# Kernel tuning notes

Measured on AMD Instinct MI355X. Metric: run time of the kernel, lower is better.

## Reference

```python
import jax, jax.numpy as jnp
import numpy as np


def setup_inputs() -> dict:
    key = jax.random.key(0)
    ks = jax.random.split(key, 8)
    Bsz, Dm, L, N = 2, 2048, 1024, 16
    u = jax.random.normal(ks[0], (Bsz, Dm, L), jnp.float32)
    delta = jax.random.normal(ks[1], (Bsz, Dm, L), jnp.float32) * 0.5
    # A is negative in Mamba (stable decay); keep values O(1) negative
    A = -jnp.exp(jax.random.normal(ks[2], (Dm, N), jnp.float32) * 0.5)
    B = jax.random.normal(ks[3], (Bsz, N, L), jnp.float32)
    C = jax.random.normal(ks[4], (Bsz, N, L), jnp.float32)
    D = jax.random.normal(ks[5], (Dm,), jnp.float32)
    z = jax.random.normal(ks[6], (Bsz, Dm, L), jnp.float32)
    delta_bias = jax.random.normal(ks[7], (Dm,), jnp.float32) * 0.1
    return {"u": u, "delta": delta, "A": A, "B": B, "C": C,
            "D": D, "z": z, "delta_bias": delta_bias, "delta_softplus": 1}


def reference(u, delta, A, B, C, D, z, delta_bias, delta_softplus):
    # u, delta, z: (Bsz, Dm, L); A: (Dm, N); B, C: (Bsz, N, L)
    dt = delta + delta_bias[None, :, None]
    if delta_softplus:
        dt = jax.nn.softplus(dt)

    # move scan (length) axis to the front
    dt_l = jnp.moveaxis(dt, -1, 0)   # (L, Bsz, Dm)
    u_l = jnp.moveaxis(u, -1, 0)     # (L, Bsz, Dm)
    B_l = jnp.moveaxis(B, -1, 0)     # (L, Bsz, N)
    C_l = jnp.moveaxis(C, -1, 0)     # (L, Bsz, N)

    def step(x, inp):
        dti, ui, Bi, Ci = inp
        dA = jnp.exp(dti[..., None] * A)                  # (Bsz, Dm, N)
        dBu = (dti * ui)[..., None] * Bi[:, None, :]      # (Bsz, Dm, N)
        x = dA * x + dBu
        y = jnp.einsum('bdn,bn->bd', x, Ci)               # (Bsz, Dm)
        return x, y

    x0 = jnp.zeros((u.shape[0], u.shape[1], A.shape[1]), dtype=u.dtype)
    _, ys = jax.lax.scan(step, x0, (dt_l, u_l, B_l, C_l))  # ys: (L, Bsz, Dm)
    y = jnp.moveaxis(ys, 0, -1)                            # (Bsz, Dm, L)
    y = y + u * D[None, :, None]
    y = y * (z * jax.nn.sigmoid(z))  # silu gate
    return y
```

## Files before the change

### kernel.cpp

```cpp
#include <hip/hip_runtime.h>
#include <math.h>

constexpr int Bsz = 2, Dm = 2048, L = 1024, N = 16;
constexpr int CL = 16;
constexpr int WPR = 2;
constexpr int RPB = 4;
constexpr int TPB = RPB * WPR * 64;
constexpr int TI = 2;
constexpr int NT = CL / TI;
constexpr int ISTR2 = 65;
constexpr int LROW2 = CL * ISTR2;
constexpr int TS2 = 8 * 65;
constexpr float LOG2E = 1.4426950408889634f;
constexpr float RLOG2E = 0.6931471805599453f;

#define EXP2(x) __builtin_amdgcn_exp2f(x)

__global__ __launch_bounds__(256) void transform_bc_kernel(
    const float* __restrict__ B_g, const float* __restrict__ C_g,
    float4* __restrict__ Bs, float4* __restrict__ Cs)
{
    const int o = threadIdx.x + 256 * blockIdx.x;
    const int b = blockIdx.y;
    const float* __restrict__ src = blockIdx.z ? C_g : B_g;
    float4* __restrict__ dst = blockIdx.z ? Cs : Bs;
    const int cg = o & 63, k = (o >> 6) & 3, i = o >> 8;
    const int l = cg * CL + i;
    float4 v;
    v.x = src[(size_t)(b * N + 4 * k + 0) * L + l];
    v.y = src[(size_t)(b * N + 4 * k + 1) * L + l];
    v.z = src[(size_t)(b * N + 4 * k + 2) * L + l];
    v.w = src[(size_t)(b * N + 4 * k + 3) * L + l];
    dst[(size_t)b * 4096 + o] = v;
}

template<bool XF>
__global__ __launch_bounds__(TPB) void mamba_scan18_kernel(
    const float* __restrict__ u_g, const float* __restrict__ delta_g,
    const float* __restrict__ A_g,
    const float* __restrict__ B_g, const float* __restrict__ C_g,
    const float4* __restrict__ Bs, const float4* __restrict__ Cs,
    const float* __restrict__ D_g, const float* __restrict__ z_g,
    const float* __restrict__ bias_g, const int* __restrict__ sp_g,
    float* __restrict__ y_g)
{
    __shared__ float2 du_s[RPB * LROW2];
    __shared__ float2 tb2[2][TI * TS2];
    __shared__ float xw_s[RPB][16];

    const int tid = threadIdx.x;
    const int wid = tid >> 6;
    const int lane = tid & 63;
    const int W = wid & 1;
    const int r = wid >> 1;
    const int h = lane >> 5;
    const int c = lane & 31;
    const int cg = W * 32 + c;
    const int row = blockIdx.x * RPB + r;
    const int b = row >> 11;
    const int d = row & (Dm - 1);
    const size_t Bb = (size_t)b * 4096;
    const int lb = r * LROW2;
    const int t128 = tid & 127;
    const int stg0 = (wid >> 2) * TS2 + (2 * (wid & 3)) * 65 + lane;
    const int stg1 = stg0 + 65;
    const int trb = (4 * h) * 65 + cg;

    float4 sB, sC;
    if (XF) sB = Bs[Bb + tid];

#pragma unroll
    for (int p = 0; p < 2; ++p) {
        const int l0 = 4 * t128 + 512 * p;
        const size_t gb = (size_t)row * L + l0;
        const float4 d4 = *reinterpret_cast<const float4*>(&delta_g[gb]);
        const float4 u4 = *reinterpret_cast<const float4*>(&u_g[gb]);
        const float bias = bias_g[d];
        const int sp = sp_g[0];
#pragma unroll
        for (int k = 0; k < 4; ++k) {
            const int li = l0 + k;
            const float t = (&d4.x)[k] + bias;
            const float e = EXP2(-fabsf(t) * LOG2E);
            const float p_ = sp ? (fmaxf(t, 0.f) +
                                   __builtin_amdgcn_logf(1.f + e) * RLOG2E)
                                : t;
            const int a = (li & (CL - 1)) * ISTR2 + (li >> 4);
            du_s[lb + a] = make_float2(p_, (&u4.x)[k]);
        }
    }
    float A2[8];
#pragma unroll
    for (int g = 0; g < 2; ++g) {
        const float4 a4 = *reinterpret_cast<const float4*>(&A_g[d * N + h * 8 + g * 4]);
        A2[g * 4 + 0] = a4.x * LOG2E; A2[g * 4 + 1] = a4.y * LOG2E;
        A2[g * 4 + 2] = a4.z * LOG2E; A2[g * 4 + 3] = a4.w * LOG2E;
    }
    if (XF) {
        tb2[0][stg0] = make_float2(sB.x, sB.y);
        tb2[0][stg1] = make_float2(sB.z, sB.w);
    }
    __syncthreads();

    float x[8], y[8];
#pragma unroll
    for (int n = 0; n < 8; ++n) { x[n] = 0.f; y[n] = 0.f; }
    float ssum = 0.f;

    if (XF) {
#pragma unroll
        for (int t = 0; t < NT; ++t) {
            if (t + 1 < NT) sB = Bs[Bb + (t + 1) * 512 + tid];
#pragma unroll
            for (int il = 0; il < TI; ++il) {
                const int i = t * TI + il;
                const float2 du = du_s[lb + i * ISTR2 + cg];
                const float dtp = du.x;
                const float dtu = du.x * du.y;
                ssum += dtp;
                const int rb = il * TS2 + trb;
                const float2 q0 = tb2[t & 1][rb];
                const float2 q1 = tb2[t & 1][rb + 65];
                const float2 q2 = tb2[t & 1][rb + 130];
                const float2 q3 = tb2[t & 1][rb + 195];
                const float bv[8] = {q0.x, q0.y, q1.x, q1.y,
                                     q2.x, q2.y, q3.x, q3.y};
#pragma unroll
                for (int n = 0; n < 8; ++n) {
                    const float a = EXP2(dtp * A2[n]);
                    x[n] = fmaf(a, x[n], dtu * bv[n]);
                }
            }
            if (t + 1 < NT) {
                tb2[(t + 1) & 1][stg0] = make_float2(sB.x, sB.y);
                tb2[(t + 1) & 1][stg1] = make_float2(sB.z, sB.w);
            }
            __syncthreads();
        }
    } else {
#pragma unroll
        for (int i = 0; i < CL; ++i) {
            const float2 du = du_s[lb + i * ISTR2 + cg];
            const float dtp = du.x;
            const float dtu = du.x * du.y;
            ssum += dtp;
            const int l = cg * CL + i;
            const int k0 = 2 * h;
            float4 B0, B1;
#pragma unroll
            for (int q = 0; q < 4; ++q) {
                (&B0.x)[q] = B_g[(size_t)(b * N + 4 * k0 + q) * L + l];
                (&B1.x)[q] = B_g[(size_t)(b * N + 4 * k0 + 4 + q) * L + l];
            }
            const float bv[8] = {B0.x, B0.y, B0.z, B0.w, B1.x, B1.y, B1.z, B1.w};
#pragma unroll
            for (int n = 0; n < 8; ++n) {
                const float a = EXP2(dtp * A2[n]);
                x[n] = fmaf(a, x[n], dtu * bv[n]);
            }
        }
    }

    if (XF) { sB = Bs[Bb + tid]; sC = Cs[Bb + tid]; }

    float P[8];
#pragma unroll
    for (int n = 0; n < 8; ++n) P[n] = EXP2(A2[n] * ssum);
#pragma unroll
    for (int s = 1; s < 32; s <<= 1) {
        const bool ok = (c >= s);
#pragma unroll
        for (int n = 0; n < 8; ++n) {
            const float xp = __shfl_up(x[n], s, 32);
            const float Pp = __shfl_up(P[n], s, 32);
            if (ok) {
                x[n] = fmaf(P[n], xp, x[n]);
                P[n] = P[n] * Pp;
            }
        }
    }

    if (W == 0 && c == 31) {
#pragma unroll
        for (int n = 0; n < 8; ++n) xw_s[r][h * 8 + n] = x[n];
    }
    if (XF) {
        tb2[0][stg0] = make_float2(sB.x, sB.y);
        tb2[0][stg1] = make_float2(sB.z, sB.w);
        tb2[1][stg0] = make_float2(sC.x, sC.y);
        tb2[1][stg1] = make_float2(sC.z, sC.w);
    }
    __syncthreads();

    float xt[8];
#pragma unroll
    for (int n = 0; n < 8; ++n) xt[n] = xw_s[r][h * 8 + n];
#pragma unroll
    for (int n = 0; n < 8; ++n) {
        const float xi = __shfl_up(x[n], 1, 32);
        const float Pi = __shfl_up(P[n], 1, 32);
        const float xe = (c == 0) ? 0.f : xi;
        const float Pe = (c == 0) ? 1.f : Pi;
        x[n] = W ? fmaf(Pe, xt[n], xe) : xe;
    }

    const float Dd = D_g[d];
    if (XF) {
#pragma unroll
        for (int t = 0; t < NT; ++t) {
            if (t + 1 < NT) {
                sB = Bs[Bb + (t + 1) * 512 + tid];
                sC = Cs[Bb + (t + 1) * 512 + tid];
            }
#pragma unroll
            for (int il = 0; il < TI; ++il) {
                const int i = t * TI + il;
                const float2 du = du_s[lb + i * ISTR2 + cg];
                const float dtp = du.x;
                const float uu = du.y;
                const float dtu = dtp * uu;
                const int rb = il * TS2 + trb;
                const float2 b0 = tb2[0][rb];
                const float2 b1 = tb2[0][rb + 65];
                const float2 b2 = tb2[0][rb + 130];
                const float2 b3 = tb2[0][rb + 195];
                const float2 c0 = tb2[1][rb];
                const float2 c1 = tb2[1][rb + 65];
                const float2 c2 = tb2[1][rb + 130];
                const float2 c3 = tb2[1][rb + 195];
                const float bv[8] = {b0.x, b0.y, b1.x, b1.y,
                                     b2.x, b2.y, b3.x, b3.y};
                const float cv[8] = {c0.x, c0.y, c1.x, c1.y,
                                     c2.x, c2.y, c3.x, c3.y};
                float acc = 0.f;
#pragma unroll
                for (int n = 0; n < 8; ++n) {
                    const float a = EXP2(dtp * A2[n]);
                    x[n] = fmaf(a, x[n], dtu * bv[n]);
                    acc = fmaf(x[n], cv[n], acc);
                }
                acc += __shfl_xor(acc, 32, 64);
                const float yv = fmaf(uu, Dd, acc);
                y[i & 7] = ((i >> 3) == h) ? yv : y[i & 7];
            }
            __syncthreads();
            if (t + 1 < NT) {
                tb2[0][stg0] = make_float2(sB.x, sB.y);
                tb2[0][stg1] = make_float2(sB.z, sB.w);
                tb2[1][stg0] = make_float2(sC.x, sC.y);
                tb2[1][stg1] = make_float2(sC.z, sC.w);
                __syncthreads();
            }
        }
    } else {
#pragma unroll
        for (int i = 0; i < CL; ++i) {
            const float2 du = du_s[lb + i * ISTR2 + cg];
            const float dtp = du.x;
            const float uu = du.y;
            const float dtu = dtp * uu;
            const int l = cg * CL + i;
            const int k0 = 2 * h;
            float4 B0, B1, C0, C1;
#pragma unroll
            for (int q = 0; q < 4; ++q) {
                (&B0.x)[q] = B_g[(size_t)(b * N + 4 * k0 + q) * L + l];
                (&B1.x)[q] = B_g[(size_t)(b * N + 4 * k0 + 4 + q) * L + l];
                (&C0.x)[q] = C_g[(size_t)(b * N + 4 * k0 + q) * L + l];
                (&C1.x)[q] = C_g[(size_t)(b * N + 4 * k0 + 4 + q) * L + l];
            }
            const float bv[8] = {B0.x, B0.y, B0.z, B0.w, B1.x, B1.y, B1.z, B1.w};
            const float cv[8] = {C0.x, C0.y, C0.z, C0.w, C1.x, C1.y, C1.z, C1.w};
            float acc = 0.f;
#pragma unroll
            for (int n = 0; n < 8; ++n) {
                const float a = EXP2(dtp * A2[n]);
                x[n] = fmaf(a, x[n], dtu * bv[n]);
                acc = fmaf(x[n], cv[n], acc);
            }
            acc += __shfl_xor(acc, 32, 64);
            const float yv = fmaf(uu, Dd, acc);
            y[i & 7] = ((i >> 3) == h) ? yv : y[i & 7];
        }
    }

    {
        const size_t gz = (size_t)row * L + cg * CL + h * 8;
        const float4 z0 = *reinterpret_cast<const float4*>(&z_g[gz]);
        const float4 z1 = *reinterpret_cast<const float4*>(&z_g[gz + 4]);
        float out[8];
#pragma unroll
        for (int j = 0; j < 8; ++j) {
            const float zv = (j < 4) ? (&z0.x)[j] : (&z1.x)[j - 4];
            const float e = EXP2(-zv * LOG2E);
            const float sig = __builtin_amdgcn_rcpf(1.f + e);
            out[j] = y[j] * (zv * sig);
        }
        *reinterpret_cast<float4*>(&y_g[gz]) =
            make_float4(out[0], out[1], out[2], out[3]);
        *reinterpret_cast<float4*>(&y_g[gz + 4]) =
            make_float4(out[4], out[5], out[6], out[7]);
    }
}

extern "C" void kernel_launch(void* const* d_in, const int* in_sizes, int n_in,
                              void* d_out, int out_size, void* d_ws, size_t ws_size,
                              hipStream_t stream) {
    const float* u     = (const float*)d_in[0];
    const float* delta = (const float*)d_in[1];
    const float* A     = (const float*)d_in[2];
    const float* B     = (const float*)d_in[3];
    const float* C     = (const float*)d_in[4];
    const float* D     = (const float*)d_in[5];
    const float* z     = (const float*)d_in[6];
    const float* bias  = (const float*)d_in[7];
    const int*   sp    = (const int*)d_in[8];
    float* y = (float*)d_out;

    const size_t bc_bytes = (size_t)Bsz * 4096 * sizeof(float4);
    const bool xf = ws_size >= 2 * bc_bytes;
    float4* Bs = (float4*)d_ws;
    float4* Cs = (float4*)((char*)d_ws + bc_bytes);

    if (xf) {
        transform_bc_kernel<<<dim3(16, Bsz, 2), 256, 0, stream>>>(B, C, Bs, Cs);
        mamba_scan18_kernel<true><<<dim3((Bsz * Dm) / RPB), TPB, 0, stream>>>(
            u, delta, A, B, C, Bs, Cs, D, z, bias, sp, y);
    } else {
        mamba_scan18_kernel<false><<<dim3((Bsz * Dm) / RPB), TPB, 0, stream>>>(
            u, delta, A, B, C, Bs, Cs, D, z, bias, sp, y);
    }
}
```

Measured before the change: 49.58 us.

## Deepen B/C prefetch pipeline and replace syncthreads with lightweight LDS barrier

Restructures the staging of the transformed B/C tiles so global loads are issued two steps ahead in registers and written into a double-buffered LDS tile, with one barrier per step instead of two. The second pass now stages B and C per timestep using half the threads each, rather than all threads loading both. A custom barrier that waits only on LDS counters (not global loads) replaces __syncthreads, so outstanding prefetches are not forced to complete at each barrier. The trade-off is more barriers in the output pass (one per timestep instead of per two) and more live registers for the prefetch buffers.

Measured after the change: 49.37 us. About the same (-0.4%).

```diff
diff --git a/kernel.cpp b/kernel.cpp
--- a/kernel.cpp
+++ b/kernel.cpp
@@ -6,8 +6,7 @@
 constexpr int WPR = 2;
 constexpr int RPB = 4;
 constexpr int TPB = RPB * WPR * 64;
-constexpr int TI = 2;
-constexpr int NT = CL / TI;
+constexpr int NT = 8;
 constexpr int ISTR2 = 65;
 constexpr int LROW2 = CL * ISTR2;
 constexpr int TS2 = 8 * 65;
@@ -15,6 +14,12 @@
 constexpr float RLOG2E = 0.6931471805599453f;
 
 #define EXP2(x) __builtin_amdgcn_exp2f(x)
+
+__device__ __forceinline__ void wg_barrier() {
+    asm volatile("s_waitcnt lgkmcnt(0)" ::: "memory");
+    __builtin_amdgcn_s_barrier();
+    asm volatile("" ::: "memory");
+}
 
 __global__ __launch_bounds__(256) void transform_bc_kernel(
     const float* __restrict__ B_g, const float* __restrict__ C_g,
@@ -35,7 +40,7 @@
 }
 
 template<bool XF>
-__global__ __launch_bounds__(TPB) void mamba_scan18_kernel(
+__global__ __launch_bounds__(TPB) void mamba_scan19_kernel(
     const float* __restrict__ u_g, const float* __restrict__ delta_g,
     const float* __restrict__ A_g,
     const float* __restrict__ B_g, const float* __restrict__ C_g,
@@ -45,7 +50,7 @@
     float* __restrict__ y_g)
 {
     __shared__ float2 du_s[RPB * LROW2];
-    __shared__ float2 tb2[2][TI * TS2];
+    __shared__ float2 tb2[2][2 * TS2];
     __shared__ float xw_s[RPB][16];
 
     const int tid = threadIdx.x;
@@ -64,29 +69,36 @@
     const int t128 = tid & 127;
     const int stg0 = (wid >> 2) * TS2 + (2 * (wid & 3)) * 65 + lane;
     const int stg1 = stg0 + 65;
+    const int bc = tid >> 8;
+    const int t256 = tid & 255;
+    const int pstg0 = bc * TS2 + (2 * ((t256 >> 6) & 3)) * 65 + (t256 & 63);
+    const int pstg1 = pstg0 + 65;
+    const float4* __restrict__ psrc = (bc ? Cs : Bs) + Bb;
     const int trb = (4 * h) * 65 + cg;
 
-    float4 sB, sC;
-    if (XF) sB = Bs[Bb + tid];
-
-#pragma unroll
-    for (int p = 0; p < 2; ++p) {
-        const int l0 = 4 * t128 + 512 * p;
-        const size_t gb = (size_t)row * L + l0;
-        const float4 d4 = *reinterpret_cast<const float4*>(&delta_g[gb]);
-        const float4 u4 = *reinterpret_cast<const float4*>(&u_g[gb]);
+    float4 s0, s1;
+    if (XF) s0 = Bs[Bb + tid];
+
+    {
         const float bias = bias_g[d];
         const int sp = sp_g[0];
 #pragma unroll
-        for (int k = 0; k < 4; ++k) {
-            const int li = l0 + k;
-            const float t = (&d4.x)[k] + bias;
-            const float e = EXP2(-fabsf(t) * LOG2E);
-            const float p_ = sp ? (fmaxf(t, 0.f) +
-                                   __builtin_amdgcn_logf(1.f + e) * RLOG2E)
-                                : t;
-            const int a = (li & (CL - 1)) * ISTR2 + (li >> 4);
-            du_s[lb + a] = make_float2(p_, (&u4.x)[k]);
+        for (int p = 0; p < 2; ++p) {
+            const int l0 = 4 * t128 + 512 * p;
+            const size_t gb = (size_t)row * L + l0;
+            const float4 d4 = *reinterpret_cast<const float4*>(&delta_g[gb]);
+            const float4 u4 = *reinterpret_cast<const float4*>(&u_g[gb]);
+#pragma unroll
+            for (int k = 0; k < 4; ++k) {
+                const int li = l0 + k;
+                const float t = (&d4.x)[k] + bias;
+                const float e = EXP2(-fabsf(t) * LOG2E);
+                const float p_ = sp ? (fmaxf(t, 0.f) +
+                                       __builtin_amdgcn_logf(1.f + e) * RLOG2E)
+                                    : t;
+                const int a = (li & (CL - 1)) * ISTR2 + (li >> 4);
+                du_s[lb + a] = make_float2(p_, (&u4.x)[k]);
+            }
         }
     }
     float A2[8];
@@ -97,10 +109,12 @@
         A2[g * 4 + 2] = a4.z * LOG2E; A2[g * 4 + 3] = a4.w * LOG2E;
     }
     if (XF) {
-        tb2[0][stg0] = make_float2(sB.x, sB.y);
-        tb2[0][stg1] = make_float2(sB.z, sB.w);
-    }
-    __syncthreads();
+        tb2[0][stg0] = make_float2(s0.x, s0.y);
+        tb2[0][stg1] = make_float2(s0.z, s0.w);
+        s0 = Bs[Bb + 512 + tid];
+        s1 = Bs[Bb + 1024 + tid];
+    }
+    wg_barrier();
 
     float x[8], y[8];
 #pragma unroll
@@ -110,10 +124,9 @@
     if (XF) {
 #pragma unroll
         for (int t = 0; t < NT; ++t) {
-            if (t + 1 < NT) sB = Bs[Bb + (t + 1) * 512 + tid];
-#pragma unroll
-            for (int il = 0; il < TI; ++il) {
-                const int i = t * TI + il;
+#pragma unroll
+            for (int il = 0; il < 2; ++il) {
+                const int i = 2 * t + il;
                 const float2 du = du_s[lb + i * ISTR2 + cg];
                 const float dtp = du.x;
                 const float dtu = du.x * du.y;
@@ -132,10 +145,15 @@
                 }
             }
             if (t + 1 < NT) {
-                tb2[(t + 1) & 1][stg0] = make_float2(sB.x, sB.y);
-                tb2[(t + 1) & 1][stg1] = make_float2(sB.z, sB.w);
-            }
-            __syncthreads();
+                const float4 sv = (t & 1) ? s1 : s0;
+                tb2[(t + 1) & 1][stg0] = make_float2(sv.x, sv.y);
+                tb2[(t + 1) & 1][stg1] = make_float2(sv.z, sv.w);
+            }
+            if (t + 3 < NT) {
+                if (t & 1) s1 = Bs[Bb + (t + 3) * 512 + tid];
+                else       s0 = Bs[Bb + (t + 3) * 512 + tid];
+            }
+            if (t + 1 < NT) wg_barrier();
         }
     } else {
 #pragma unroll
@@ -161,7 +179,8 @@
         }
     }
 
-    if (XF) { sB = Bs[Bb + tid]; sC = Cs[Bb + tid]; }
+    float4 p0, p1;
+    if (XF) p0 = psrc[t256];
 
     float P[8];
 #pragma unroll
@@ -185,12 +204,12 @@
         for (int n = 0; n < 8; ++n) xw_s[r][h * 8 + n] = x[n];
     }
     if (XF) {
-        tb2[0][stg0] = make_float2(sB.x, sB.y);
-        tb2[0][stg1] = make_float2(sB.z, sB.w);
-        tb2[1][stg0] = make_float2(sC.x, sC.y);
-        tb2[1][stg1] = make_float2(sC.z, sC.w);
-    }
-    __syncthreads();
+        tb2[0][pstg0] = make_float2(p0.x, p0.y);
+        tb2[0][pstg1] = make_float2(p0.z, p0.w);
+        p0 = psrc[1 * 256 + t256];
+        p1 = psrc[2 * 256 + t256];
+    }
+    wg_barrier();
 
     float xt[8];
 #pragma unroll
@@ -207,50 +226,41 @@
     const float Dd = D_g[d];
     if (XF) {
 #pragma unroll
-        for (int t = 0; t < NT; ++t) {
-            if (t + 1 < NT) {
-                sB = Bs[Bb + (t + 1) * 512 + tid];
-                sC = Cs[Bb + (t + 1) * 512 + tid];
-            }
-#pragma unroll
-            for (int il = 0; il < TI; ++il) {
-                const int i = t * TI + il;
-                const float2 du = du_s[lb + i * ISTR2 + cg];
-                const float dtp = du.x;
-                const float uu = du.y;
-                const float dtu = dtp * uu;
-                const int rb = il * TS2 + trb;
-                const float2 b0 = tb2[0][rb];
-                const float2 b1 = tb2[0][rb + 65];
-                const float2 b2 = tb2[0][rb + 130];
-                const float2 b3 = tb2[0][rb + 195];
-                const float2 c0 = tb2[1][rb];
-                const float2 c1 = tb2[1][rb + 65];
-                const float2 c2 = tb2[1][rb + 130];
-                const float2 c3 = tb2[1][rb + 195];
-                const float bv[8] = {b0.x, b0.y, b1.x, b1.y,
-                                     b2.x, b2.y, b3.x, b3.y};
-                const float cv[8] = {c0.x, c0.y, c1.x, c1.y,
-                                     c2.x, c2.y, c3.x, c3.y};
-                float acc = 0.f;
-#pragma unroll
-                for (int n = 0; n < 8; ++n) {
-                    const float a = EXP2(dtp * A2[n]);
-                    x[n] = fmaf(a, x[n], dtu * bv[n]);
-                    acc = fmaf(x[n], cv[n], acc);
-                }
-                acc += __shfl_xor(acc, 32, 64);
-                const float yv = fmaf(uu, Dd, acc);
-                y[i & 7] = ((i >> 3) == h) ? yv : y[i & 7];
-            }
-            __syncthreads();
-            if (t + 1 < NT) {
-                tb2[0][stg0] = make_float2(sB.x, sB.y);
-                tb2[0][stg1] = make_float2(sB.z, sB.w);
-                tb2[1][stg0] = make_float2(sC.x, sC.y);
-                tb2[1][stg1] = make_float2(sC.z, sC.w);
-                __syncthreads();
-            }
+        for (int i = 0; i < CL; ++i) {
+            const float2 du = du_s[lb + i * ISTR2 + cg];
+            const float dtp = du.x;
+            const float uu = du.y;
+            const float dtu = dtp * uu;
+            const float2 b0 = tb2[i & 1][trb];
+            const float2 b1 = tb2[i & 1][trb + 65];
+            const float2 b2 = tb2[i & 1][trb + 130];
+            const float2 b3 = tb2[i & 1][trb + 195];
+            const float2 c0 = tb2[i & 1][TS2 + trb];
+            const float2 c1 = tb2[i & 1][TS2 + trb + 65];
+            const float2 c2 = tb2[i & 1][TS2 + trb + 130];
+            const float2 c3 = tb2[i & 1][TS2 + trb + 195];
+            const float bv[8] = {b0.x, b0.y, b1.x, b1.y, b2.x, b2.y, b3.x, b3.y};
+            const float cv[8] = {c0.x, c0.y, c1.x, c1.y, c2.x, c2.y, c3.x, c3.y};
+            float acc = 0.f;
+#pragma unroll
+            for (int n = 0; n < 8; ++n) {
+                const float a = EXP2(dtp * A2[n]);
+                x[n] = fmaf(a, x[n], dtu * bv[n]);
+                acc = fmaf(x[n], cv[n], acc);
+            }
+            acc += __shfl_xor(acc, 32, 64);
+            const float yv = fmaf(uu, Dd, acc);
+            y[i & 7] = ((i >> 3) == h) ? yv : y[i & 7];
+            if (i + 1 < CL) {
+                const float4 pv = (i & 1) ? p1 : p0;
+                tb2[(i + 1) & 1][pstg0] = make_float2(pv.x, pv.y);
+                tb2[(i + 1) & 1][pstg1] = make_float2(pv.z, pv.w);
+            }
+            if (i + 3 < CL) {
+                if (i & 1) p1 = psrc[(i + 3) * 256 + t256];
+                else       p0 = psrc[(i + 3) * 256 + t256];
+            }
+            if (i + 1 < CL) wg_barrier();
         }
     } else {
 #pragma unroll
@@ -324,10 +334,10 @@
 
     if (xf) {
         transform_bc_kernel<<<dim3(16, Bsz, 2), 256, 0, stream>>>(B, C, Bs, Cs);
-        mamba_scan18_kernel<true><<<dim3((Bsz * Dm) / RPB), TPB, 0, stream>>>(
+        mamba_scan19_kernel<true><<<dim3((Bsz * Dm) / RPB), TPB, 0, stream>>>(
             u, delta, A, B, C, Bs, Cs, D, z, bias, sp, y);
     } else {
-        mamba_scan18_kernel<false><<<dim3((Bsz * Dm) / RPB), TPB, 0, stream>>>(
+        mamba_scan19_kernel<false><<<dim3((Bsz * Dm) / RPB), TPB, 0, stream>>>(
             u, delta, A, B, C, Bs, Cs, D, z, bias, sp, y);
     }
 }
```
